# Performance work log

Hardware: AMD Instinct MI355X
Metric: run time of the kernel (lower is better)

## Reference

```python
import math
import jax, jax.numpy as jnp
import numpy as np

P = 8; K = 9; RC = 8; FC = 768; TOPK = 2
THR = 0.2; TEMP = 0.08; DIL = 5; MIX = 0.65; OPEN = 5


def _build_bank():
    axis = np.linspace(-1.0, 1.0, K, dtype=np.float32)
    yy, xx = np.meshgrid(axis, axis, indexing='ij')
    Ls = [0.45, 0.75, 1.05]; Ws = [0.14, 0.2, 0.28]
    kernels, oris, lens, wids = [], [], [], []
    for i in range(P):
        ang = 2.0 * math.pi * i / P
        L = Ls[i % 3]; W = Ws[(i // 3) % 3]
        xr = xx * math.cos(ang) + yy * math.sin(ang)
        yr = -xx * math.sin(ang) + yy * math.cos(ang)
        taper = (1.0 - np.clip(np.abs(xr) / L, 0.0, 1.0)) ** 1.5
        core = np.exp(-0.5 * ((xr / L) ** 2 + (yr / W) ** 2))
        ridge = taper * core * np.clip(1.0 - (yr / W) ** 2, 0.0, None)
        k = ridge - ridge.mean()
        k = k / max(np.abs(k).sum(), 1e-6)
        kernels.append(k.astype(np.float32)); oris.append(ang); lens.append(L); wids.append(W)
    return (jnp.asarray(np.stack(kernels)[:, None]),
            jnp.asarray(np.array(oris, np.float32)),
            jnp.asarray(np.array(lens, np.float32)),
            jnp.asarray(np.array(wids, np.float32)))


def _conv(x, w, b, pad):
    y = jax.lax.conv_general_dilated(x, w, (1, 1), [(pad, pad), (pad, pad)],
                                     dimension_numbers=('NCHW', 'OIHW', 'NCHW'))
    return y + b[None, :, None, None]


def _avg3(x):  # torch avg_pool2d k=3,s=1,p=1 with count_include_pad=True -> sum/9
    s = jax.lax.reduce_window(x, 0.0, jax.lax.add, (1, 1, 3, 3), (1, 1, 1, 1),
                              [(0, 0), (0, 0), (1, 1), (1, 1)])
    return s / 9.0


def _maxp(x, k):
    p = k // 2
    return jax.lax.reduce_window(x, -jnp.inf, jax.lax.max, (1, 1, k, k), (1, 1, 1, 1),
                                 [(0, 0), (0, 0), (p, p), (p, p)])


def _binary_open(mask, k):
    eroded = 1.0 - _maxp(1.0 - mask, k)
    return jnp.clip(_maxp(eroded, k), 0.0, 1.0)


def _normalize(t):
    mn = t.min(axis=(-2, -1), keepdims=True)
    mx = t.max(axis=(-2, -1), keepdims=True)
    return (t - mn) / jnp.maximum(mx - mn, 1e-6)


def _gelu(x):
    return jax.nn.gelu(x, approximate=False)


def _forward(feature_map, theta, length, width, curvature, alpha, objectness,
             prototype_logits, fp1_w, fp1_b, fp2_w, fp2_b, pm1_w, pm1_b,
             pm2_w, pm2_b, proto_delta):
    bank, ori, la, wa = _build_bank()
    carrier = _gelu(_conv(_gelu(_conv(feature_map, fp1_w, fp1_b, 0)), fp2_w, fp2_b, 1))
    carrier_mean = carrier.mean(axis=1, keepdims=True)
    carrier_hp = carrier_mean - _avg3(carrier_mean)
    kernels = bank + 0.05 * proto_delta
    responses = jax.lax.conv_general_dilated(carrier_hp, kernels, (1, 1),
                                             [(K // 2, K // 2)] * 2,
                                             dimension_numbers=('NCHW', 'OIHW', 'NCHW'))
    theta_angle = jnp.tanh(theta) * math.pi  # [B,1,H,W]
    theta_score = jnp.cos(theta_angle - ori[None, :, None, None])
    length_value = jax.nn.sigmoid(length) * 0.85 + 0.25
    width_value = jax.nn.sigmoid(width) * 0.22 + 0.08
    length_score = -(length_value - la[None, :, None, None]) ** 2 / 0.08
    width_score = -(width_value - wa[None, :, None, None]) ** 2 / 0.01
    bias = prototype_logits + 1.25 * theta_score + length_score + width_score
    pw = jax.nn.softmax(bias, axis=1)  # [B,P,H,W]
    # per-pixel top-k prototype selection
    pwt = jnp.moveaxis(pw, 1, -1)  # [B,H,W,P]
    vals, idx = jax.lax.top_k(pwt, TOPK)
    sparse = (jax.nn.one_hot(idx, P, dtype=pw.dtype) * vals[..., None]).sum(axis=-2)
    sparse = sparse / jnp.maximum(sparse.sum(axis=-1, keepdims=True), 1e-6)
    pw = jnp.moveaxis(sparse, -1, 1)
    alpha_map = jax.nn.sigmoid(alpha)
    objectness_map = jax.nn.sigmoid(objectness)
    curvature_map = jnp.tanh(curvature)
    ss = (responses * pw).sum(axis=1, keepdims=True)
    ss = ss - _avg3(ss)
    density = jnp.abs(carrier).mean(axis=1, keepdims=True)
    density = density / jnp.maximum(density.mean(axis=(2, 3), keepdims=True), 1e-6)
    dx = jnp.cos(theta_angle); dy = jnp.sin(theta_angle)
    blob = _avg3(objectness_map)
    # support gating (enabled, hard-mask + opening)
    carrier_support = _normalize(_avg3(jnp.abs(carrier_hp)))
    density_support = _normalize(density)
    ev = MIX * carrier_support + (1.0 - MIX) * density_support
    gate = jax.nn.sigmoid((ev - THR) / TEMP)
    gate = _maxp(gate, DIL)
    mask = (ev >= THR).astype(feature_map.dtype)
    mask = _binary_open(mask, OPEN)
    mask = _maxp(mask, DIL)
    gate = gate * mask
    blob = blob * jax.lax.stop_gradient(gate)
    stroke_gate = alpha_map * blob * (0.7 + 0.3 * jnp.clip(density, 0.0, 2.0))
    ss = stroke_gate * ss * (1.0 + 0.15 * curvature_map)
    feats = jnp.concatenate([carrier * ss, ss, dx * ss, dy * ss, curvature_map * ss], axis=1)  # [B,RC+4,H,W]
    h = _gelu(_conv(feats, pm1_w, pm1_b, 0))
    return _conv(h, pm2_w, pm2_b, 0)  # [B,FC,H,W]


def setup_inputs() -> dict:
    key = jax.random.key(0)
    ks = jax.random.split(key, 16)
    B, H, W = 8, 64, 64
    n = lambda k, s: jax.random.normal(k, s, dtype=jnp.float32)
    return {
        'feature_map': n(ks[0], (B, FC, H, W)),
        'theta': n(ks[1], (B, 1, H, W)),
        'length': n(ks[2], (B, 1, H, W)),
        'width': n(ks[3], (B, 1, H, W)),
        'curvature': n(ks[4], (B, 1, H, W)),
        'alpha': n(ks[5], (B, 1, H, W)),
        'objectness': n(ks[6], (B, 1, H, W)),
        'prototype_logits': n(ks[7], (B, P, H, W)),
        'fp1_w': n(ks[8], (RC, FC, 1, 1)) * 0.02,
        'fp1_b': jnp.zeros((RC,), jnp.float32),
        'fp2_w': n(ks[9], (RC, RC, 3, 3)) * 0.05,
        'fp2_b': jnp.zeros((RC,), jnp.float32),
        'pm1_w': n(ks[10], (RC, RC + 4, 1, 1)) * 0.05,
        'pm1_b': jnp.zeros((RC,), jnp.float32),
        'pm2_w': n(ks[11], (FC, RC, 1, 1)) * 0.05,
        'pm2_b': jnp.zeros((FC,), jnp.float32),
        'proto_delta': n(ks[12], (P, 1, K, K)) * 0.02,
    }


def reference(feature_map, theta, length, width, curvature, alpha, objectness,
              prototype_logits, fp1_w, fp1_b, fp2_w, fp2_b, pm1_w, pm1_b,
              pm2_w, pm2_b, proto_delta):
    return _forward(feature_map, theta, length, width, curvature, alpha, objectness,
                    prototype_logits, fp1_w, fp1_b, fp2_w, fp2_b, pm1_w, pm1_b,
                    pm2_w, pm2_b, proto_delta)
```

## Files before the change

### kernel.cpp

```cpp
#include <hip/hip_runtime.h>
#include <math.h>

#define PI_F 3.14159265358979323846f

__device__ __forceinline__ float gelu_f(float x){ return 0.5f*x*(1.0f+erff(x*0.7071067811865475f)); }
__device__ __forceinline__ float sigm_f(float x){ return 1.0f/(1.0f+expf(-x)); }

typedef float nf4 __attribute__((ext_vector_type(4)));
__device__ __forceinline__ float4 nt_load4(const float4* p){
    nf4 v = __builtin_nontemporal_load((const nf4*)p);
    return make_float4(v.x, v.y, v.z, v.w);
}
__device__ __forceinline__ void nt_store4(float4* p, float4 v){
    nf4 w; w.x=v.x; w.y=v.y; w.z=v.z; w.w=v.w;
    __builtin_nontemporal_store(w, (nf4*)p);
}


__global__ void __launch_bounds__(256) k_conv1(const float* __restrict__ fm,
                        const float* __restrict__ w1, const float* __restrict__ b1,
                        const float* __restrict__ pd,
                        float* __restrict__ t1, float* __restrict__ klg){
    __shared__ float wl[768*8];
    __shared__ float4 pT[16][8][16];
    int bln = blockIdx.x;
    int tid = threadIdx.x;
    int b = bln>>6;
    int q4base = (bln&63)<<4;
    for (int i=tid;i<6144;i+=256){ int c=i>>3, co=i&7; wl[i]=w1[co*768 + c]; }
    __syncthreads();
    int f4i = tid&15, grp = tid>>4;
    int q4 = q4base + f4i;
    const float4* fm4 = (const float4*)fm;
    float4 acc[8];
    #pragma unroll
    for(int co=0;co<8;co++) acc[co]=make_float4(0.f,0.f,0.f,0.f);
    int ch0 = grp*48;
    #pragma unroll 4
    for(int c=0;c<48;c++){
        int ch = ch0 + c;
        float4 x = nt_load4(&fm4[(size_t)(b*768 + ch)*1024 + q4]);
        #pragma unroll
        for(int co=0;co<8;co++){
            float wv = wl[(ch<<3)+co];
            acc[co].x += wv*x.x; acc[co].y += wv*x.y; acc[co].z += wv*x.z; acc[co].w += wv*x.w;
        }
    }
    #pragma unroll
    for(int co=0;co<8;co++) pT[grp][co][f4i]=acc[co];
    __syncthreads();
    if(tid<128){
        int co=tid>>4, fi=tid&15;
        float4 s=make_float4(0.f,0.f,0.f,0.f);
        #pragma unroll
        for(int g=0;g<16;g++){
            float4 v=pT[g][co][fi];
            s.x+=v.x; s.y+=v.y; s.z+=v.z; s.w+=v.w;
        }
        float bb=b1[co];
        float4 o;
        o.x=gelu_f(s.x+bb); o.y=gelu_f(s.y+bb); o.z=gelu_f(s.z+bb); o.w=gelu_f(s.w+bb);
        ((float4*)t1)[(size_t)co*8192 + (b<<10) + q4base + fi] = o;
    }

    if(bln==0){
        __shared__ float ridge[648];
        __shared__ float pmS[8], pdenS[8];
        for(int t=tid;t<648;t+=256){
            int p=t/81, idx=t-p*81;
            int i=idx/9, j=idx-i*9;
            float ay=-1.f+0.25f*(float)i;
            float ax=-1.f+0.25f*(float)j;
            float ang=2.f*PI_F*(float)p*0.125f;
            const float Ls[3]={0.45f,0.75f,1.05f};
            const float Ws[3]={0.14f,0.20f,0.28f};
            float L=Ls[p%3], Wd=Ws[(p/3)%3];
            float cs=cosf(ang), sn=sinf(ang);
            float xr=ax*cs+ay*sn;
            float yr=-ax*sn+ay*cs;
            float tp=1.f-fminf(fabsf(xr)/L,1.f);
            float taper=powf(tp,1.5f);
            float core=expf(-0.5f*((xr/L)*(xr/L)+(yr/Wd)*(yr/Wd)));
            ridge[t]=taper*core*fmaxf(1.f-(yr/Wd)*(yr/Wd),0.f);
        }
        __syncthreads();
        {
            int p=tid>>5, k=tid&31;
            float s=0.f;
            for(int e=k;e<81;e+=32) s+=ridge[p*81+e];
            for(int off=16;off>0;off>>=1) s+=__shfl_down(s,off,32);
            if(k==0) pmS[p]=s*(1.f/81.f);
        }
        __syncthreads();
        {
            int p=tid>>5, k=tid&31;
            float m=pmS[p];
            float s=0.f;
            for(int e=k;e<81;e+=32) s+=fabsf(ridge[p*81+e]-m);
            for(int off=16;off>0;off>>=1) s+=__shfl_down(s,off,32);
            if(k==0) pdenS[p]=fmaxf(s,1e-6f);
        }
        __syncthreads();
        for(int t=tid;t<648;t+=256){
            int p=t/81;
            klg[t]=(ridge[t]-pmS[p])/pdenS[p]+0.05f*pd[t];
        }
    }
}

__global__ void __launch_bounds__(256) k_conv2(const float* __restrict__ t1,
    const float* __restrict__ w2, const float* __restrict__ b2,
    float* __restrict__ carrier, float* __restrict__ cm, float* __restrict__ absc,
    float* __restrict__ bpart){
    __shared__ float t1T[8][3][64];
    __shared__ float w2s[576];
    __shared__ float sumS[4][64];
    __shared__ float saS[4][64];
    int tid=threadIdx.x, bl=blockIdx.x;
    int b=bl>>6, y=bl&63;
    for(int i=tid;i<576;i+=256) w2s[i]=w2[i];
    for(int j=tid;j<1536;j+=256){
        int ci=j/192, rem=j-ci*192, r=rem>>6, x=rem&63;
        int gy=y-1+r;
        float v=0.f;
        if(gy>=0 && gy<64){
            v = t1[(size_t)ci*32768 + (b<<12)+(gy<<6)+x];
        }
        t1T[ci][r][x]=v;
    }
    __syncthreads();
    int x=tid&63, cg=tid>>6;
    float acc[2];
    #pragma unroll
    for(int qq=0;qq<2;qq++) acc[qq]=b2[cg*2+qq];
    for(int ci=0;ci<8;ci++){
        #pragma unroll
        for(int r=0;r<3;r++){
            #pragma unroll
            for(int dx=-1;dx<=1;dx++){
                int xx=x+dx;
                float v=(xx>=0&&xx<64)?t1T[ci][r][xx]:0.f;
                int ti=r*3+(dx+1);
                #pragma unroll
                for(int qq=0;qq<2;qq++) acc[qq]+=v*w2s[(((cg*2+qq)*8+ci)*9)+ti];
            }
        }
    }
    float s2=0.f, sa2=0.f;
    #pragma unroll
    for(int qq=0;qq<2;qq++){
        float cv=gelu_f(acc[qq]);
        carrier[((size_t)((b<<3)+cg*2+qq)<<12)+(y<<6)+x]=cv;
        s2+=cv; sa2+=fabsf(cv);
    }
    sumS[cg][x]=s2; saS[cg][x]=sa2;
    __syncthreads();
    if(cg==0){
        float cmv=(sumS[0][x]+sumS[1][x]+sumS[2][x]+sumS[3][x])*0.125f;
        float av =(saS[0][x]+saS[1][x]+saS[2][x]+saS[3][x])*0.125f;
        int gp=(b<<12)+(y<<6)+x;
        cm[gp]=cmv;
        absc[gp]=av;
        float s=av, mn=av, mx=av;
        #pragma unroll
        for(int off=32;off>0;off>>=1){
            s += __shfl_down(s,off);
            mn = fminf(mn,__shfl_down(mn,off));
            mx = fmaxf(mx,__shfl_down(mx,off));
        }
        if(x==0){
            bpart[bl*8+0]=s;
            bpart[bl*8+3]=mn;
            bpart[bl*8+4]=mx;
        }
    }
}

__global__ void __launch_bounds__(256) k_resp(const float* __restrict__ cm,
    const float* __restrict__ klg, const float* __restrict__ theta,
    const float* __restrict__ length, const float* __restrict__ width,
    const float* __restrict__ plog,
    float* __restrict__ csraw, float* __restrict__ ss0, float* __restrict__ bpart){
    __shared__ float cmT[704];
    __shared__ float chpT[576];
    __shared__ float klS[648];
    __shared__ float mg[64][16];
    int tid=threadIdx.x, bl=blockIdx.x;
    int b=bl>>6, y=bl&63;
    for(int i=tid;i<648;i+=256) klS[i]=klg[i];
    for(int j=tid;j<704;j+=256){
        int r=j>>6, x=j&63;
        int gy=y-5+r;
        cmT[j]=(gy>=0&&gy<64)?cm[(b<<12)+(gy<<6)+x]:0.f;
    }
    __syncthreads();
    for(int j=tid;j<576;j+=256){
        int rh=j>>6, x=j&63;
        int gy=y-4+rh;
        float v=0.f;
        if(gy>=0&&gy<64){
            float s=0.f;
            #pragma unroll
            for(int dy=0;dy<3;dy++){
                #pragma unroll
                for(int dx=-1;dx<=1;dx++){
                    int xx=x+dx;
                    if(xx>=0&&xx<64) s+=cmT[(rh+dy)*64+xx];
                }
            }
            v=cmT[(rh+1)*64+x]-s*(1.f/9.f);
        }
        chpT[j]=v;
    }
    __syncthreads();
    int x=tid&63, qg=tid>>6;
    int gp=(b<<12)+(y<<6)+x;
    float acc[2]={0.f,0.f};
    float cs=0.f;
    for(int dy=-4;dy<=4;dy++){
        int lr=dy+4;
        for(int dx=-4;dx<=4;dx++){
            int xx=x+dx;
            float v=(xx>=0&&xx<64)?chpT[lr*64+xx]:0.f;
            int ti=lr*9+(dx+4);
            acc[0]+=v*klS[(qg*2)*81+ti];
            acc[1]+=v*klS[(qg*2+1)*81+ti];
            if(qg==0 && dy>=-1&&dy<=1&&dx>=-1&&dx<=1) cs+=fabsf(v);
        }
    }
    float ta=tanhf(theta[gp])*PI_F;
    float lv=sigm_f(length[gp])*0.85f+0.25f;
    float wv=sigm_f(width[gp])*0.22f+0.08f;
    const float Ls[3]={0.45f,0.75f,1.05f};
    const float Ws[3]={0.14f,0.20f,0.28f};
    int pp=(y<<6)+x;
    float bias[2];
    #pragma unroll
    for(int qq=0;qq<2;qq++){
        int q=qg*2+qq;
        float ang=2.f*PI_F*(float)q*0.125f;
        float la=Ls[q%3], wa=Ws[(q/3)%3];
        bias[qq]=plog[((size_t)((b<<3)+q)<<12)+pp]
               +1.25f*cosf(ta-ang)
               -(lv-la)*(lv-la)*(1.f/0.08f)
               -(wv-wa)*(wv-wa)*(1.f/0.01f);
    }
    float m1,r1,m2,r2;
    if(bias[1]>bias[0]){ m1=bias[1];r1=acc[1]; m2=bias[0];r2=acc[0]; }
    else               { m1=bias[0];r1=acc[0]; m2=bias[1];r2=acc[1]; }
    mg[x][qg*4+0]=m1; mg[x][qg*4+1]=r1; mg[x][qg*4+2]=m2; mg[x][qg*4+3]=r2;
    __syncthreads();
    if(qg==0){
        float M1=mg[x][0],R1=mg[x][1],M2=mg[x][2],R2=mg[x][3];
        #pragma unroll
        for(int g=1;g<4;g++){
            float m1b=mg[x][g*4],r1b=mg[x][g*4+1],m2b=mg[x][g*4+2],r2b=mg[x][g*4+3];
            if(m1b>M1){
                float nM2,nR2;
                if(m2b>M1){nM2=m2b;nR2=r2b;} else {nM2=M1;nR2=R1;}
                M1=m1b;R1=r1b;M2=nM2;R2=nR2;
            } else if(m1b>M2){
                M2=m1b;R2=r1b;
            }
        }
        float e2=expf(M2-M1);
        float inv=1.0f/(1.0f+e2);
        ss0[gp]=R1*inv + R2*e2*inv;
        float csv=cs*(1.f/9.f);
        csraw[gp]=csv;
        float mn=csv, mx=csv;
        #pragma unroll
        for(int off=32;off>0;off>>=1){
            mn=fminf(mn,__shfl_down(mn,off));
            mx=fmaxf(mx,__shfl_down(mx,off));
        }
        if(x==0){
            bpart[bl*8+1]=mn;
            bpart[bl*8+2]=mx;
        }
    }
}

__global__ void __launch_bounds__(256) k_out(const float* __restrict__ ss0,
    const float* __restrict__ csraw, const float* __restrict__ absc,
    const float* __restrict__ objn, const float* __restrict__ alpha,
    const float* __restrict__ theta, const float* __restrict__ curv,
    const float* __restrict__ carrier, const float* __restrict__ bpart,
    const float* __restrict__ w3, const float* __restrict__ b3,
    const float* __restrict__ w4, const float* __restrict__ b4,
    float* __restrict__ out){
    __shared__ float hS[8][64];
    __shared__ float w4s[768*8];
    __shared__ float b4s[768];
    __shared__ float wl3[96];
    __shared__ float bl3[8];
    __shared__ float evT[13*64];
    __shared__ float gmT[13*64];
    __shared__ float eT[9*64];
    __shared__ float m1T[5*64];
    __shared__ float obT[3*64];
    __shared__ float red5[5];
    int tid=threadIdx.x;
    int bln=blockIdx.x;
    int b=bln>>6, y=bln&63;
    for(int i=tid;i<6144;i+=256) w4s[i]=w4[i];
    for(int i=tid;i<768;i+=256) b4s[i]=b4[i];
    if(tid<96) wl3[tid]=w3[tid];
    if(tid<8) bl3[tid]=b3[tid];
    if(tid<64){
        const float* bp=&bpart[((size_t)b*64+tid)*8];
        float sm=bp[0], cmn=bp[1], cmx=bp[2], amn=bp[3], amx=bp[4];
        #pragma unroll
        for(int off=32;off>0;off>>=1){
            sm  += __shfl_down(sm,off);
            cmn  = fminf(cmn,__shfl_down(cmn,off));
            cmx  = fmaxf(cmx,__shfl_down(cmx,off));
            amn  = fminf(amn,__shfl_down(amn,off));
            amx  = fmaxf(amx,__shfl_down(amx,off));
        }
        if(tid==0){
            float den=fmaxf(sm*(1.0f/4096.0f),1e-6f);
            red5[0]=den; red5[1]=cmn; red5[2]=cmx; red5[3]=amn/den; red5[4]=amx/den;
        }
    }
    __syncthreads();
    float den=red5[0], cmn=red5[1], dmn=red5[3];
    float cinv = 1.0f/fmaxf(red5[2]-cmn,1e-6f);
    float dinv = 1.0f/fmaxf(red5[4]-dmn,1e-6f);
    for(int j=tid;j<832;j+=256){
        int r=j>>6, x=j&63; int gy=y-6+r;
        float ev=0.f;
        if(gy>=0&&gy<64){
            int gp=(b<<12)+(gy<<6)+x;
            float cs=(csraw[gp]-cmn)*cinv;
            float d=absc[gp]/den;
            ev=0.65f*cs+0.35f*((d-dmn)*dinv);
        }
        evT[j]=ev;
        gmT[j]=sigm_f((ev-0.2f)*(1.0f/0.08f));
    }
    for(int j=tid;j<192;j+=256){
        int r=j>>6,x=j&63; int gy=y-1+r;
        obT[j]=(gy>=0&&gy<64)?sigm_f(objn[(b<<12)+(gy<<6)+x]):0.f;
    }
    __syncthreads();
    for(int j=tid;j<576;j+=256){
        int r=j>>6,x=j&63; int gy=y-4+r;
        float m=0.f;
        if(gy>=0&&gy<64){
            m=1.f;
            for(int dy=-2;dy<=2;dy++){int yy=gy+dy; if(yy<0||yy>=64)continue;
                int lr=yy-(y-6);
                for(int dx=-2;dx<=2;dx++){int xx=x+dx; if(xx<0||xx>=64)continue;
                    if(evT[(lr<<6)+xx]<0.2f) m=0.f;}}
        }
        eT[j]=m;
    }
    __syncthreads();
    for(int j=tid;j<320;j+=256){
        int r=j>>6,x=j&63; int gy=y-2+r;
        float m=0.f;
        if(gy>=0&&gy<64){
            m=-1e30f;
            for(int dy=-2;dy<=2;dy++){int yy=gy+dy; if(yy<0||yy>=64)continue;
                int lr=yy-(y-4);
                for(int dx=-2;dx<=2;dx++){int xx=x+dx; if(xx<0||xx>=64)continue;
                    m=fmaxf(m,eT[(lr<<6)+xx]);}}
        }
        m1T[j]=m;
    }
    __syncthreads();
    if(tid<64){
        int x=tid;
        int gp=(b<<12)+(y<<6)+x;
        float m2=-1e30f, gx=-1e30f;
        for(int dy=-2;dy<=2;dy++){int yy=y+dy; if(yy<0||yy>=64)continue;
            int lr1=yy-(y-2), lr2=yy-(y-6);
            for(int dx=-2;dx<=2;dx++){int xx=x+dx; if(xx<0||xx>=64)continue;
                m2=fmaxf(m2,m1T[(lr1<<6)+xx]);
                gx=fmaxf(gx,gmT[(lr2<<6)+xx]);}}
        float s=0.f;
        for(int dy=-1;dy<=1;dy++){int yy=y+dy; if(yy<0||yy>=64)continue;
            int lr=yy-(y-1);
            for(int dx=-1;dx<=1;dx++){int xx=x+dx; if(xx<0||xx>=64)continue;
                s+=obT[(lr<<6)+xx];}}
        float blob=s*(1.0f/9.0f);
        float gate=gx*m2;
        float d=absc[gp]/den;
        float sgv=sigm_f(alpha[gp])*blob*gate*(0.7f+0.3f*fminf(fmaxf(d,0.f),2.f));
        const float* base = ss0 + (b<<12);
        float ssum=0.f;
        for(int dy=-1;dy<=1;dy++){int yy=y+dy; if(yy<0||yy>=64)continue;
            for(int dx=-1;dx<=1;dx++){int xx=x+dx;if(xx<0||xx>=64)continue;
                ssum+=base[(yy<<6)+xx];}}
        float ss1 = base[(y<<6)+x]-ssum*(1.0f/9.0f);
        float cu = tanhf(curv[gp]);
        float ssv = sgv*ss1*(1.0f+0.15f*cu);
        float ta = tanhf(theta[gp])*PI_F;
        float dxv=cosf(ta), dyv=sinf(ta);
        float car[8];
        #pragma unroll
        for(int ci=0;ci<8;ci++) car[ci]=carrier[((size_t)((b<<3)+ci)<<12)+(y<<6)+x];
        #pragma unroll
        for(int co=0;co<8;co++){
            const float* w=&wl3[co*12];
            float t = w[8] + w[9]*dxv + w[10]*dyv + w[11]*cu;
            #pragma unroll
            for(int ci=0;ci<8;ci++) t += w[ci]*car[ci];
            hS[co][tid] = gelu_f(bl3[co] + ssv*t);
        }
    }
    __syncthreads();
    int px4 = tid&15;
    int cg = tid>>4;
    int q0 = bln*16 + px4;
    int bb_ = q0>>10;
    int ql = q0 & 1023;
    float4 hv[8];
    #pragma unroll
    for(int ci=0;ci<8;ci++) hv[ci]=*(const float4*)&hS[ci][px4<<2];
    float4* o4=(float4*)out;
    for(int k=0;k<48;k++){
        int co=cg*48+k;
        float bv=b4s[co];
        float4 o=make_float4(bv,bv,bv,bv);
        const float* w=&w4s[co<<3];
        #pragma unroll
        for(int ci=0;ci<8;ci++){
            float wv=w[ci];
            o.x+=wv*hv[ci].x; o.y+=wv*hv[ci].y; o.z+=wv*hv[ci].z; o.w+=wv*hv[ci].w;
        }
        nt_store4(&o4[(size_t)(bb_*768+co)*1024 + ql], o);
    }
}

extern "C" void kernel_launch(void* const* d_in, const int* in_sizes, int n_in,
                              void* d_out, int out_size, void* d_ws, size_t ws_size,
                              hipStream_t stream) {
    const float* fm     =(const float*)d_in[0];
    const float* theta  =(const float*)d_in[1];
    const float* length =(const float*)d_in[2];
    const float* width  =(const float*)d_in[3];
    const float* curv   =(const float*)d_in[4];
    const float* alpha  =(const float*)d_in[5];
    const float* objn   =(const float*)d_in[6];
    const float* plog   =(const float*)d_in[7];
    const float* fp1w   =(const float*)d_in[8];
    const float* fp1b   =(const float*)d_in[9];
    const float* fp2w   =(const float*)d_in[10];
    const float* fp2b   =(const float*)d_in[11];
    const float* pm1w   =(const float*)d_in[12];
    const float* pm1b   =(const float*)d_in[13];
    const float* pm2w   =(const float*)d_in[14];
    const float* pm2b   =(const float*)d_in[15];
    const float* pdelta =(const float*)d_in[16];

    float* ws=(float*)d_ws;
    float* t1      = ws;
    float* carrier = t1 + 262144;
    float* absc    = carrier + 262144;
    float* csraw   = absc + 32768;
    float* ss0     = csraw + 32768;
    float* cm      = ss0 + 32768;
    float* bpart   = cm + 32768;
    float* klg     = bpart + 4096;
    float* out     = (float*)d_out;

    k_conv1<<<512, 256, 0, stream>>>(fm, fp1w, fp1b, pdelta, t1, klg);
    k_conv2<<<512, 256, 0, stream>>>(t1, fp2w, fp2b, carrier, cm, absc, bpart);
    k_resp <<<512, 256, 0, stream>>>(cm, klg, theta, length, width, plog,
                                     csraw, ss0, bpart);
    k_out  <<<512, 256, 0, stream>>>(ss0, csraw, absc, objn, alpha, theta, curv,
                                     carrier, bpart, pm1w, pm1b, pm2w, pm2b, out);
}
```

Baseline: 246.0 us.

## Fuse conv2 and response kernels, recomputing conv2 halo rows per block

Merges the 3x3 conv2+GELU kernel into the response kernel. Each block now loads 13 rows of t1 and recomputes the 11 channel-mean rows its 9x9 stencil needs, so the cm intermediate buffer and one launch go away. The cost is about 11x redundant conv2 work per block (all 8 output channels across 704 positions) and a larger shared-memory footprint, which may reduce occupancy.

New measurement: 351.4 us. +42.8%, slower.

```diff
diff --git a/kernel.cpp b/kernel.cpp
--- a/kernel.cpp
+++ b/kernel.cpp
@@ -108,90 +108,68 @@
     }
 }
 
-__global__ void __launch_bounds__(256) k_conv2(const float* __restrict__ t1,
+__global__ void __launch_bounds__(256) k_mid(const float* __restrict__ t1,
     const float* __restrict__ w2, const float* __restrict__ b2,
-    float* __restrict__ carrier, float* __restrict__ cm, float* __restrict__ absc,
-    float* __restrict__ bpart){
-    __shared__ float t1T[8][3][64];
-    __shared__ float w2s[576];
-    __shared__ float sumS[4][64];
-    __shared__ float saS[4][64];
-    int tid=threadIdx.x, bl=blockIdx.x;
-    int b=bl>>6, y=bl&63;
-    for(int i=tid;i<576;i+=256) w2s[i]=w2[i];
-    for(int j=tid;j<1536;j+=256){
-        int ci=j/192, rem=j-ci*192, r=rem>>6, x=rem&63;
-        int gy=y-1+r;
-        float v=0.f;
-        if(gy>=0 && gy<64){
-            v = t1[(size_t)ci*32768 + (b<<12)+(gy<<6)+x];
-        }
-        t1T[ci][r][x]=v;
-    }
-    __syncthreads();
-    int x=tid&63, cg=tid>>6;
-    float acc[2];
-    #pragma unroll
-    for(int qq=0;qq<2;qq++) acc[qq]=b2[cg*2+qq];
-    for(int ci=0;ci<8;ci++){
-        #pragma unroll
-        for(int r=0;r<3;r++){
-            #pragma unroll
-            for(int dx=-1;dx<=1;dx++){
-                int xx=x+dx;
-                float v=(xx>=0&&xx<64)?t1T[ci][r][xx]:0.f;
-                int ti=r*3+(dx+1);
-                #pragma unroll
-                for(int qq=0;qq<2;qq++) acc[qq]+=v*w2s[(((cg*2+qq)*8+ci)*9)+ti];
-            }
-        }
-    }
-    float s2=0.f, sa2=0.f;
-    #pragma unroll
-    for(int qq=0;qq<2;qq++){
-        float cv=gelu_f(acc[qq]);
-        carrier[((size_t)((b<<3)+cg*2+qq)<<12)+(y<<6)+x]=cv;
-        s2+=cv; sa2+=fabsf(cv);
-    }
-    sumS[cg][x]=s2; saS[cg][x]=sa2;
-    __syncthreads();
-    if(cg==0){
-        float cmv=(sumS[0][x]+sumS[1][x]+sumS[2][x]+sumS[3][x])*0.125f;
-        float av =(saS[0][x]+saS[1][x]+saS[2][x]+saS[3][x])*0.125f;
-        int gp=(b<<12)+(y<<6)+x;
-        cm[gp]=cmv;
-        absc[gp]=av;
-        float s=av, mn=av, mx=av;
-        #pragma unroll
-        for(int off=32;off>0;off>>=1){
-            s += __shfl_down(s,off);
-            mn = fminf(mn,__shfl_down(mn,off));
-            mx = fmaxf(mx,__shfl_down(mx,off));
-        }
-        if(x==0){
-            bpart[bl*8+0]=s;
-            bpart[bl*8+3]=mn;
-            bpart[bl*8+4]=mx;
-        }
-    }
-}
-
-__global__ void __launch_bounds__(256) k_resp(const float* __restrict__ cm,
     const float* __restrict__ klg, const float* __restrict__ theta,
     const float* __restrict__ length, const float* __restrict__ width,
     const float* __restrict__ plog,
+    float* __restrict__ carrier, float* __restrict__ absc,
     float* __restrict__ csraw, float* __restrict__ ss0, float* __restrict__ bpart){
-    __shared__ float cmT[704];
-    __shared__ float chpT[576];
+    __shared__ float t1T[13][8][64];
+    __shared__ float w2s[576];
+    __shared__ float cmT[11][64];
+    __shared__ float absS[64];
+    __shared__ float chpT[9][64];
     __shared__ float klS[648];
     __shared__ float mg[64][16];
     int tid=threadIdx.x, bl=blockIdx.x;
     int b=bl>>6, y=bl&63;
+    for(int i=tid;i<576;i+=256) w2s[i]=w2[i];
     for(int i=tid;i<648;i+=256) klS[i]=klg[i];
+    for(int j=tid;j<6656;j+=256){
+        int rr=j>>9, rem=j&511, ci=rem>>6, x=rem&63;
+        int gy=y-6+rr;
+        float v=0.f;
+        if(gy>=0&&gy<64) v=t1[(size_t)ci*32768+(b<<12)+(gy<<6)+x];
+        t1T[rr][ci][x]=v;
+    }
+    __syncthreads();
     for(int j=tid;j<704;j+=256){
         int r=j>>6, x=j&63;
         int gy=y-5+r;
-        cmT[j]=(gy>=0&&gy<64)?cm[(b<<12)+(gy<<6)+x]:0.f;
+        float cmv=0.f;
+        if(gy>=0&&gy<64){
+            float acc[8];
+            #pragma unroll
+            for(int co=0;co<8;co++) acc[co]=b2[co];
+            for(int ci=0;ci<8;ci++){
+                #pragma unroll
+                for(int dr=0;dr<3;dr++){
+                    #pragma unroll
+                    for(int dx=-1;dx<=1;dx++){
+                        int xx=x+dx;
+                        float v=(xx>=0&&xx<64)?t1T[r+dr][ci][xx]:0.f;
+                        int ti=dr*3+(dx+1);
+                        #pragma unroll
+                        for(int co=0;co<8;co++) acc[co]+=v*w2s[(co*8+ci)*9+ti];
+                    }
+                }
+            }
+            float s=0.f, sa=0.f;
+            #pragma unroll
+            for(int co=0;co<8;co++){
+                float cv=gelu_f(acc[co]);
+                s+=cv; sa+=fabsf(cv);
+                if(r==5) carrier[((size_t)((b<<3)+co)<<12)+(y<<6)+x]=cv;
+            }
+            cmv=s*0.125f;
+            if(r==5){
+                float av=sa*0.125f;
+                absc[(b<<12)+(y<<6)+x]=av;
+                absS[x]=av;
+            }
+        }
+        cmT[r][x]=cmv;
     }
     __syncthreads();
     for(int j=tid;j<576;j+=256){
@@ -205,26 +183,26 @@
                 #pragma unroll
                 for(int dx=-1;dx<=1;dx++){
                     int xx=x+dx;
-                    if(xx>=0&&xx<64) s+=cmT[(rh+dy)*64+xx];
+                    if(xx>=0&&xx<64) s+=cmT[rh+dy][xx];
                 }
             }
-            v=cmT[(rh+1)*64+x]-s*(1.f/9.f);
-        }
-        chpT[j]=v;
+            v=cmT[rh+1][x]-s*(1.f/9.f);
+        }
+        chpT[rh][x]=v;
     }
     __syncthreads();
     int x=tid&63, qg=tid>>6;
     int gp=(b<<12)+(y<<6)+x;
-    float acc[2]={0.f,0.f};
+    float acc2[2]={0.f,0.f};
     float cs=0.f;
     for(int dy=-4;dy<=4;dy++){
         int lr=dy+4;
         for(int dx=-4;dx<=4;dx++){
             int xx=x+dx;
-            float v=(xx>=0&&xx<64)?chpT[lr*64+xx]:0.f;
+            float v=(xx>=0&&xx<64)?chpT[lr][xx]:0.f;
             int ti=lr*9+(dx+4);
-            acc[0]+=v*klS[(qg*2)*81+ti];
-            acc[1]+=v*klS[(qg*2+1)*81+ti];
+            acc2[0]+=v*klS[(qg*2)*81+ti];
+            acc2[1]+=v*klS[(qg*2+1)*81+ti];
             if(qg==0 && dy>=-1&&dy<=1&&dx>=-1&&dx<=1) cs+=fabsf(v);
         }
     }
@@ -246,8 +224,8 @@
                -(wv-wa)*(wv-wa)*(1.f/0.01f);
     }
     float m1,r1,m2,r2;
-    if(bias[1]>bias[0]){ m1=bias[1];r1=acc[1]; m2=bias[0];r2=acc[0]; }
-    else               { m1=bias[0];r1=acc[0]; m2=bias[1];r2=acc[1]; }
+    if(bias[1]>bias[0]){ m1=bias[1];r1=acc2[1]; m2=bias[0];r2=acc2[0]; }
+    else               { m1=bias[0];r1=acc2[0]; m2=bias[1];r2=acc2[1]; }
     mg[x][qg*4+0]=m1; mg[x][qg*4+1]=r1; mg[x][qg*4+2]=m2; mg[x][qg*4+3]=r2;
     __syncthreads();
     if(qg==0){
@@ -268,15 +246,22 @@
         ss0[gp]=R1*inv + R2*e2*inv;
         float csv=cs*(1.f/9.f);
         csraw[gp]=csv;
-        float mn=csv, mx=csv;
+        float av=absS[x];
+        float sm=av, amn=av, amx=av, cmn=csv, cmx=csv;
         #pragma unroll
         for(int off=32;off>0;off>>=1){
-            mn=fminf(mn,__shfl_down(mn,off));
-            mx=fmaxf(mx,__shfl_down(mx,off));
+            sm  += __shfl_down(sm,off);
+            amn  = fminf(amn,__shfl_down(amn,off));
+            amx  = fmaxf(amx,__shfl_down(amx,off));
+            cmn  = fminf(cmn,__shfl_down(cmn,off));
+            cmx  = fmaxf(cmx,__shfl_down(cmx,off));
         }
         if(x==0){
-            bpart[bl*8+1]=mn;
-            bpart[bl*8+2]=mx;
+            bpart[bl*8+0]=sm;
+            bpart[bl*8+1]=cmn;
+            bpart[bl*8+2]=cmx;
+            bpart[bl*8+3]=amn;
+            bpart[bl*8+4]=amx;
         }
     }
 }
@@ -461,15 +446,13 @@
     float* absc    = carrier + 262144;
     float* csraw   = absc + 32768;
     float* ss0     = csraw + 32768;
-    float* cm      = ss0 + 32768;
-    float* bpart   = cm + 32768;
+    float* bpart   = ss0 + 32768;
     float* klg     = bpart + 4096;
     float* out     = (float*)d_out;
 
     k_conv1<<<512, 256, 0, stream>>>(fm, fp1w, fp1b, pdelta, t1, klg);
-    k_conv2<<<512, 256, 0, stream>>>(t1, fp2w, fp2b, carrier, cm, absc, bpart);
-    k_resp <<<512, 256, 0, stream>>>(cm, klg, theta, length, width, plog,
-                                     csraw, ss0, bpart);
+    k_mid  <<<512, 256, 0, stream>>>(t1, fp2w, fp2b, klg, theta, length, width, plog,
+                                     carrier, absc, csraw, ss0, bpart);
     k_out  <<<512, 256, 0, stream>>>(ss0, csraw, absc, objn, alpha, theta, curv,
                                      carrier, bpart, pm1w, pm1b, pm2w, pm2b, out);
 }
```
